# Kernel optimization log

Measured on AMD Instinct MI355X. Metric: run time of the kernel, lower is better.

Reference implementation:

```python
import jax, jax.numpy as jnp
import numpy as np

EPS = 1e-16

def setup_inputs() -> dict:
    key = jax.random.key(0)
    k1, k2, k3, k4, k5, k6 = jax.random.split(key, 6)
    B, S, NT, E = 8, 256, 50, 64
    # sorted event times in [0, 90); horizon T = 100 > all events; all valid (>=0)
    event_times = jnp.sort(jax.random.uniform(k1, (B, S), dtype=jnp.float32) * 90.0, axis=1)
    event_types = jax.random.randint(k2, (B, S), 0, NT)
    # parameters initialized N(0, 0.1) as in _initialize_parameters
    type_embeddings = 0.1 * jax.random.normal(k3, (NT, E), dtype=jnp.float32)
    a = 0.1 * jax.random.normal(k4, (NT, E), dtype=jnp.float32)
    A = 0.1 * jax.random.normal(k5, (NT, NT, E), dtype=jnp.float32)
    P = 0.1 * jax.random.normal(k6, (NT, NT, E), dtype=jnp.float32)
    return {"event_times": event_times, "event_types": event_types, "T": 100,
            "type_embeddings": type_embeddings, "a": a, "A": A, "P": P}

def _hawkes_nll(event_times, event_types, T, emb, a, A, P):
    B, S = event_times.shape
    NT, E = emb.shape
    Tf = jnp.asarray(T, jnp.float32)
    emb_t = emb[event_types]            # (B,S,E) embedding of each event's type
    a_t = a[event_types]                # (B,S,E)
    valid = event_times >= 0.0          # (B,S)

    # ---- log-likelihood: intensity of the observed type at each event time ----
    # pairwise: axis 1 = query event i, axis 2 = history event j (j < i)
    dt = event_times[:, :, None] - event_times[:, None, :]                 # (B,Si,Sj)
    hist_mask = (jnp.arange(S)[:, None] > jnp.arange(S)[None, :])[None]    # (1,Si,Sj): j<i
    # A_pair[b,i,j,e] = A[type_j, type_i, e]; same for P_pair
    A_pair = A[event_types[:, None, :], event_types[:, :, None]]           # (B,Si,Sj,E)
    P_pair = P[event_types[:, None, :], event_types[:, :, None]]
    emb_i = emb_t[:, :, None, :]                                           # (B,Si,1,E)
    emb_j = emb_t[:, None, :, :]                                           # (B,1,Sj,E)
    decay = jnp.exp(-(emb_i * P_pair) * emb_j * dt[..., None])
    contrib = (emb_i * A_pair) * decay * emb_j                             # (B,Si,Sj,E)
    m = jnp.sum(jnp.where(hist_mask[..., None], contrib, 0.0), axis=2)     # (B,Si,E)
    inten = jnp.sum(jax.nn.softplus(emb_t * a_t + m), axis=-1)             # (B,S)
    ll = jnp.sum(jnp.where(valid, jnp.log(inten + EPS), 0.0))

    # ---- integral approximation (as in compute_loss) ----
    # intensity at horizon T for ALL types, using full valid history
    dT = Tf - event_times                                                  # (B,S)
    A_all = A[event_types]                                                 # (B,S,NT,E): A[t_j, t, e]
    P_all = P[event_types]
    decT = jnp.exp(-(emb[None, None] * P_all) * emb_t[:, :, None, :] * dT[:, :, None, None])
    conT = (emb[None, None] * A_all) * decT * emb_t[:, :, None, :]         # (B,S,NT,E)
    m_T = jnp.sum(jnp.where(valid[:, :, None, None], conT, 0.0), axis=1)   # (B,NT,E)
    inten_T = jnp.sum(jax.nn.softplus(emb * a + m_T), axis=(-2, -1))       # (B,)

    base_sum = jnp.sum(jax.nn.softplus(emb * a))                           # empty-history intensity summed over types
    any_valid = jnp.any(valid, axis=1)                                     # (B,)
    last_time = jnp.where(any_valid, jnp.max(jnp.where(valid, event_times, -1e30), axis=1), 0.0)
    first_time = jnp.where(any_valid, jnp.min(jnp.where(valid, event_times, 1e30), axis=1), 0.0)
    integ_b = jnp.where(any_valid,
                        inten_T * (Tf - last_time) + base_sum * first_time,
                        base_sum * Tf)
    integral = jnp.sum(integ_b)
    return -(ll - integral)

def reference(event_times, event_types, T, type_embeddings, a, A, P):
    return _hawkes_nll(event_times, event_types, T, type_embeddings, a, A, P)
```

## Files before the change

### kernel.cpp

```cpp
#include <hip/hip_runtime.h>
#include <math.h>

#define B   8
#define S   256
#define NT  50
#define E   64
#define EPSF 1e-16f

#define NW        4
#define LL_BLOCKS (B * S / 2)
#define IN_BLOCKS (B * NT)

__device__ __forceinline__ float softplus(float x) {
    if (x > 20.0f) return x;
    return log1pf(__expf(x));
}

__device__ __forceinline__ float wave_reduce_sum(float v) {
    #pragma unroll
    for (int off = 32; off > 0; off >>= 1)
        v += __shfl_down(v, off, 64);
    return v;
}

__global__ __launch_bounds__(64 * NW) void main_kernel(
    const float* __restrict__ times, const int* __restrict__ types,
    const int* __restrict__ Tp,
    const float* __restrict__ emb,  const float* __restrict__ a,
    const float* __restrict__ Amat, const float* __restrict__ Pmat,
    float* __restrict__ ws_ll, float* __restrict__ ws_int)
{
    const int tid = threadIdx.x;
    const int e   = tid & 63;
    const int w   = tid >> 6;
    const int bid = blockIdx.x;
    const bool is_ll = (bid < LL_BLOCKS);
    const int b = is_ll ? (bid / (S / 2)) : ((bid - LL_BLOCKS) / NT);

    __shared__ float s_emb[NT * E];
    __shared__ float s_t[S];
    __shared__ int   s_ty[S];
    __shared__ float s_part[2][NW][E];
    __shared__ float s_row[2];

    for (int idx = tid; idx < NT * E; idx += 64 * NW)
        s_emb[idx] = emb[idx];
    for (int j = tid; j < S; j += 64 * NW) {
        s_t[j]  = times[b * S + j];
        s_ty[j] = types[b * S + j];
    }
    __syncthreads();

    if (is_ll) {
        const int ih = bid % (S / 2);
        const int rows[2] = { ih, S - 1 - ih };
        #pragma unroll
        for (int r = 0; r < 2; ++r) {
            const int   i     = rows[r];
            const float t_i   = s_t[i];
            const int   ty_i  = s_ty[i];
            const float emb_i = s_emb[ty_i * E + e];
            float m = 0.0f;
            #pragma unroll 4
            for (int j = w; j < i; j += NW) {
                const int   ty_j = s_ty[j];
                const float dt   = t_i - s_t[j];
                const int   base = (ty_j * NT + ty_i) * E + e;
                const float embj = s_emb[ty_j * E + e];
                m += emb_i * Amat[base] * __expf(-emb_i * Pmat[base] * embj * dt) * embj;
            }
            s_part[r][w][e] = m;
        }
        __syncthreads();
        if (w < 2) {
            const int   i     = rows[w];
            const float t_i   = s_t[i];
            const int   ty_i  = s_ty[i];
            const float emb_i = s_emb[ty_i * E + e];
            float mt = 0.0f;
            #pragma unroll
            for (int q = 0; q < NW; ++q) mt += s_part[w][q][e];
            const float sp    = softplus(emb_i * a[ty_i * E + e] + mt);
            const float inten = wave_reduce_sum(sp);
            if (e == 0)
                s_row[w] = (t_i >= 0.0f) ? logf(inten + EPSF) : 0.0f;
        }
        __syncthreads();
        if (tid == 0) ws_ll[bid] = s_row[0] + s_row[1];
    } else {
        const int   k    = (bid - LL_BLOCKS) % NT;
        const float Tf   = (float)(*Tp);
        const float embk = s_emb[k * E + e];
        float mT = 0.0f;
        #pragma unroll 4
        for (int i = w; i < S; i += NW) {
            const float t_i  = s_t[i];
            const int   ty   = s_ty[i];
            const float embt = s_emb[ty * E + e];
            const int   idx  = (ty * NT + k) * E + e;
            const float c = embk * Amat[idx]
                          * __expf(-embk * Pmat[idx] * embt * (Tf - t_i)) * embt;
            mT += (t_i >= 0.0f) ? c : 0.0f;
        }
        s_part[0][w][e] = mT;
        __syncthreads();
        if (w == 0) {
            float mt = 0.0f;
            #pragma unroll
            for (int q = 0; q < NW; ++q) mt += s_part[0][q][e];
            const float sp = softplus(embk * a[k * E + e] + mt);
            const float s  = wave_reduce_sum(sp);
            if (e == 0) ws_int[bid - LL_BLOCKS] = s;
        }
    }
}

__global__ __launch_bounds__(256) void finalize_kernel(
    const float* __restrict__ times,
    const int* __restrict__ Tp,
    const float* __restrict__ emb, const float* __restrict__ a,
    const float* __restrict__ ws_ll, const float* __restrict__ ws_int,
    float* __restrict__ out)
{
    const int t = threadIdx.x;
    const float Tf = (float)(*Tp);

    float llp = 0.0f;
    for (int idx = t; idx < LL_BLOCKS; idx += 256) llp += ws_ll[idx];
    float bs = 0.0f;
    for (int idx = t; idx < NT * E; idx += 256) bs += softplus(emb[idx] * a[idx]);

    __shared__ float red[256], red2[256];
    red[t] = llp; red2[t] = bs;
    __syncthreads();
    for (int off = 128; off > 0; off >>= 1) {
        if (t < off) { red[t] += red[t + off]; red2[t] += red2[t + off]; }
        __syncthreads();
    }
    __shared__ float s_ll, s_base;
    if (t == 0) { s_ll = red[0]; s_base = red2[0]; }
    __syncthreads();
    const float base_sum = s_base;

    __shared__ float s_intenT[B];
    {
        const int bb   = t >> 5;
        const int lane = t & 31;
        float v = 0.0f;
        for (int k = lane; k < NT; k += 32) v += ws_int[bb * NT + k];
        #pragma unroll
        for (int off = 16; off > 0; off >>= 1)
            v += __shfl_down(v, off, 32);
        if (lane == 0) s_intenT[bb] = v;
    }
    __syncthreads();

    __shared__ float rmin[256], rmax[256];
    __shared__ float s_integral;
    if (t == 0) s_integral = 0.0f;
    __syncthreads();

    for (int b = 0; b < B; ++b) {
        const float tv = times[b * S + t];
        const bool valid = (tv >= 0.0f);
        rmin[t] = valid ? tv : 1e30f;
        rmax[t] = valid ? tv : -1e30f;
        __syncthreads();
        for (int off = 128; off > 0; off >>= 1) {
            if (t < off) {
                rmin[t] = fminf(rmin[t], rmin[t + off]);
                rmax[t] = fmaxf(rmax[t], rmax[t + off]);
            }
            __syncthreads();
        }
        if (t == 0) {
            const bool any_valid = (rmin[0] < 1e29f);
            const float first = any_valid ? rmin[0] : 0.0f;
            const float last  = any_valid ? rmax[0] : 0.0f;
            const float ib = any_valid
                ? s_intenT[b] * (Tf - last) + base_sum * first
                : base_sum * Tf;
            s_integral += ib;
        }
        __syncthreads();
    }

    if (t == 0)
        out[0] = s_integral - s_ll;
}

extern "C" void kernel_launch(void* const* d_in, const int* in_sizes, int n_in,
                              void* d_out, int out_size, void* d_ws, size_t ws_size,
                              hipStream_t stream) {
    const float* times = (const float*)d_in[0];
    const int*   types = (const int*)d_in[1];
    const int*   Tp    = (const int*)d_in[2];
    const float* emb   = (const float*)d_in[3];
    const float* a     = (const float*)d_in[4];
    const float* Amat  = (const float*)d_in[5];
    const float* Pmat  = (const float*)d_in[6];

    float* ws     = (float*)d_ws;
    float* ws_ll  = ws;
    float* ws_int = ws + LL_BLOCKS;
    float* out    = (float*)d_out;

    main_kernel<<<LL_BLOCKS + IN_BLOCKS, 64 * NW, 0, stream>>>(
        times, types, Tp, emb, a, Amat, Pmat, ws_ll, ws_int);
    finalize_kernel<<<1, 256, 0, stream>>>(times, Tp, emb, a, ws_ll, ws_int, out);
}
```

Baseline: 98.40 us.

## Pack event arrays, vectorize embedding load, simplify inner math, streamline finalize reduction

Packs event times and types into one float2 shared array and loads the embedding table with float4. It hoists the negated query embedding, moves the emb_i multiply out of the inner sum into the softplus argument, and raises unroll from 4 to 8. The finalize kernel replaces the serial per-batch block-wide min/max reductions with wave-shuffle reductions spread over waves, which cuts many barriers. The main cost, gathered A/P global loads, is unchanged, so gains depend mainly on instruction count and finalize latency.

```diff
diff --git a/kernel.cpp b/kernel.cpp
--- a/kernel.cpp
+++ b/kernel.cpp
@@ -5,6 +5,7 @@
 #define S   256
 #define NT  50
 #define E   64
+#define NTE (NT * E)
 #define EPSF 1e-16f
 
 #define NW        4
@@ -37,18 +38,19 @@
     const bool is_ll = (bid < LL_BLOCKS);
     const int b = is_ll ? (bid / (S / 2)) : ((bid - LL_BLOCKS) / NT);
 
-    __shared__ float s_emb[NT * E];
-    __shared__ float s_t[S];
-    __shared__ int   s_ty[S];
-    __shared__ float s_part[2][NW][E];
-    __shared__ float s_row[2];
-
-    for (int idx = tid; idx < NT * E; idx += 64 * NW)
-        s_emb[idx] = emb[idx];
-    for (int j = tid; j < S; j += 64 * NW) {
-        s_t[j]  = times[b * S + j];
-        s_ty[j] = types[b * S + j];
-    }
+    __shared__ __align__(16) float s_emb[NTE];
+    __shared__ float2 s_ev[S];
+    __shared__ float  s_part[2][NW][E];
+    __shared__ float  s_row[2];
+
+    {
+        const float4* __restrict__ emb4 = (const float4*)emb;
+        float4* s4 = (float4*)s_emb;
+        for (int idx = tid; idx < NTE / 4; idx += 64 * NW)
+            s4[idx] = emb4[idx];
+    }
+    for (int j = tid; j < S; j += 64 * NW)
+        s_ev[j] = make_float2(times[b * S + j], __int_as_float(types[b * S + j]));
     __syncthreads();
 
     if (is_ll) {
@@ -57,30 +59,36 @@
         #pragma unroll
         for (int r = 0; r < 2; ++r) {
             const int   i     = rows[r];
-            const float t_i   = s_t[i];
-            const int   ty_i  = s_ty[i];
-            const float emb_i = s_emb[ty_i * E + e];
-            float m = 0.0f;
-            #pragma unroll 4
+            const float t_i   = s_ev[i].x;
+            const int   ty_i  = __float_as_int(s_ev[i].y);
+            const int   col   = ty_i * E + e;
+            const float negEi = -s_emb[col];
+
+            float macc = 0.0f;
+            #pragma unroll 8
             for (int j = w; j < i; j += NW) {
-                const int   ty_j = s_ty[j];
-                const float dt   = t_i - s_t[j];
-                const int   base = (ty_j * NT + ty_i) * E + e;
-                const float embj = s_emb[ty_j * E + e];
-                m += emb_i * Amat[base] * __expf(-emb_i * Pmat[base] * embj * dt) * embj;
+                const float2 ev  = s_ev[j];
+                const int   tyj  = __float_as_int(ev.y);
+                const float dtj  = t_i - ev.x;
+                const int   base = tyj * NTE + col;
+                const float ej   = s_emb[tyj * E + e];
+                const float Pe   = Pmat[base];
+                const float Ae   = Amat[base];
+                macc = fmaf(Ae * ej, __expf(negEi * Pe * ej * dtj), macc);
             }
-            s_part[r][w][e] = m;
+            s_part[r][w][e] = macc;
         }
         __syncthreads();
         if (w < 2) {
             const int   i     = rows[w];
-            const float t_i   = s_t[i];
-            const int   ty_i  = s_ty[i];
-            const float emb_i = s_emb[ty_i * E + e];
+            const float t_i   = s_ev[i].x;
+            const int   ty_i  = __float_as_int(s_ev[i].y);
+            const int   col   = ty_i * E + e;
+            const float emb_i = s_emb[col];
             float mt = 0.0f;
             #pragma unroll
             for (int q = 0; q < NW; ++q) mt += s_part[w][q][e];
-            const float sp    = softplus(emb_i * a[ty_i * E + e] + mt);
+            const float sp    = softplus(fmaf(emb_i, mt, emb_i * a[col]));
             const float inten = wave_reduce_sum(sp);
             if (e == 0)
                 s_row[w] = (t_i >= 0.0f) ? logf(inten + EPSF) : 0.0f;
@@ -90,25 +98,28 @@
     } else {
         const int   k    = (bid - LL_BLOCKS) % NT;
         const float Tf   = (float)(*Tp);
-        const float embk = s_emb[k * E + e];
-        float mT = 0.0f;
-        #pragma unroll 4
+        const int   colk = k * E + e;
+        const float embk = s_emb[colk];
+        const float negEk = -embk;
+
+        float acc = 0.0f;
+        #pragma unroll 8
         for (int i = w; i < S; i += NW) {
-            const float t_i  = s_t[i];
-            const int   ty   = s_ty[i];
-            const float embt = s_emb[ty * E + e];
-            const int   idx  = (ty * NT + k) * E + e;
-            const float c = embk * Amat[idx]
-                          * __expf(-embk * Pmat[idx] * embt * (Tf - t_i)) * embt;
-            mT += (t_i >= 0.0f) ? c : 0.0f;
-        }
-        s_part[0][w][e] = mT;
+            const float2 ev  = s_ev[i];
+            const int   ty   = __float_as_int(ev.y);
+            const float dT   = Tf - ev.x;
+            const int   base = ty * NTE + colk;
+            const float et   = s_emb[ty * E + e];
+            const float c    = Amat[base] * et * __expf(negEk * Pmat[base] * et * dT);
+            acc += (ev.x >= 0.0f) ? c : 0.0f;
+        }
+        s_part[0][w][e] = acc;
         __syncthreads();
         if (w == 0) {
             float mt = 0.0f;
             #pragma unroll
             for (int q = 0; q < NW; ++q) mt += s_part[0][q][e];
-            const float sp = softplus(embk * a[k * E + e] + mt);
+            const float sp = softplus(fmaf(embk, mt, embk * a[colk]));
             const float s  = wave_reduce_sum(sp);
             if (e == 0) ws_int[bid - LL_BLOCKS] = s;
         }
@@ -122,71 +133,62 @@
     const float* __restrict__ ws_ll, const float* __restrict__ ws_int,
     float* __restrict__ out)
 {
-    const int t = threadIdx.x;
+    const int t    = threadIdx.x;
+    const int lane = t & 63;
+    const int w    = t >> 6;
     const float Tf = (float)(*Tp);
 
     float llp = 0.0f;
     for (int idx = t; idx < LL_BLOCKS; idx += 256) llp += ws_ll[idx];
     float bs = 0.0f;
-    for (int idx = t; idx < NT * E; idx += 256) bs += softplus(emb[idx] * a[idx]);
+    for (int idx = t; idx < NTE; idx += 256) bs += softplus(emb[idx] * a[idx]);
 
     __shared__ float red[256], red2[256];
     red[t] = llp; red2[t] = bs;
+
+    __shared__ float s_first[B], s_last[B], s_iT[B], s_any[B];
+    for (int b = w; b < B; b += 4) {
+        float mn = 1e30f, mx = -1e30f;
+        #pragma unroll
+        for (int q = 0; q < S / 64; ++q) {
+            const float tv = times[b * S + q * 64 + lane];
+            const bool valid = (tv >= 0.0f);
+            mn = fminf(mn, valid ? tv : 1e30f);
+            mx = fmaxf(mx, valid ? tv : -1e30f);
+        }
+        float iv = (lane < NT) ? ws_int[b * NT + lane] : 0.0f;
+        #pragma unroll
+        for (int off = 32; off > 0; off >>= 1) {
+            mn = fminf(mn, __shfl_down(mn, off, 64));
+            mx = fmaxf(mx, __shfl_down(mx, off, 64));
+            iv += __shfl_down(iv, off, 64);
+        }
+        if (lane == 0) {
+            const bool any_valid = (mn < 1e29f);
+            s_any[b]   = any_valid ? 1.0f : 0.0f;
+            s_first[b] = any_valid ? mn : 0.0f;
+            s_last[b]  = any_valid ? mx : 0.0f;
+            s_iT[b]    = iv;
+        }
+    }
     __syncthreads();
+
     for (int off = 128; off > 0; off >>= 1) {
         if (t < off) { red[t] += red[t + off]; red2[t] += red2[t + off]; }
         __syncthreads();
     }
-    __shared__ float s_ll, s_base;
-    if (t == 0) { s_ll = red[0]; s_base = red2[0]; }
-    __syncthreads();
-    const float base_sum = s_base;
-
-    __shared__ float s_intenT[B];
-    {
-        const int bb   = t >> 5;
-        const int lane = t & 31;
-        float v = 0.0f;
-        for (int k = lane; k < NT; k += 32) v += ws_int[bb * NT + k];
-        #pragma unroll
-        for (int off = 16; off > 0; off >>= 1)
-            v += __shfl_down(v, off, 32);
-        if (lane == 0) s_intenT[bb] = v;
-    }
-    __syncthreads();
-
-    __shared__ float rmin[256], rmax[256];
-    __shared__ float s_integral;
-    if (t == 0) s_integral = 0.0f;
-    __syncthreads();
-
-    for (int b = 0; b < B; ++b) {
-        const float tv = times[b * S + t];
-        const bool valid = (tv >= 0.0f);
-        rmin[t] = valid ? tv : 1e30f;
-        rmax[t] = valid ? tv : -1e30f;
-        __syncthreads();
-        for (int off = 128; off > 0; off >>= 1) {
-            if (t < off) {
-                rmin[t] = fminf(rmin[t], rmin[t + off]);
-                rmax[t] = fmaxf(rmax[t], rmax[t + off]);
-            }
-            __syncthreads();
-        }
-        if (t == 0) {
-            const bool any_valid = (rmin[0] < 1e29f);
-            const float first = any_valid ? rmin[0] : 0.0f;
-            const float last  = any_valid ? rmax[0] : 0.0f;
-            const float ib = any_valid
-                ? s_intenT[b] * (Tf - last) + base_sum * first
+
+    if (t == 0) {
+        const float base_sum = red2[0];
+        float integral = 0.0f;
+        #pragma unroll
+        for (int b = 0; b < B; ++b) {
+            integral += (s_any[b] > 0.5f)
+                ? s_iT[b] * (Tf - s_last[b]) + base_sum * s_first[b]
                 : base_sum * Tf;
-            s_integral += ib;
-        }
-        __syncthreads();
-    }
-
-    if (t == 0)
-        out[0] = s_integral - s_ll;
+        }
+        out[0] = integral - red[0];
+    }
 }
 
 extern "C" void kernel_launch(void* const* d_in, const int* in_sizes, int n_in,
```

Result: faster. 89.44 us (-9.1%).
